# Performance work log

Measured on AMD Instinct MI355X. Metric: run time of the kernel, lower is better.

Reference implementation:

```python
import jax, jax.numpy as jnp
import numpy as np

B, S, D, H = 2, 2048, 1024, 16  # batch, pad_size, depth, num_heads
HD = D // H


def setup_inputs() -> dict:
    key = jax.random.key(0)
    ks = jax.random.split(key, 20)
    g = lambda k, shape, fan: jax.random.normal(k, shape, jnp.float32) * np.sqrt(2.0 / fan)
    return {
        "x": jax.random.normal(ks[0], (B, S, D), jnp.float32),
        "W_in": g(ks[1], (D, D), 2 * D), "b_in": g(ks[2], (D,), D),
        "Wq": g(ks[3], (D, D), 2 * D), "bq": g(ks[4], (D,), D),
        "Wk": g(ks[5], (D, D), 2 * D), "bk": g(ks[6], (D,), D),
        "Wv": g(ks[7], (D, D), 2 * D), "bv": g(ks[8], (D,), D),
        "Wo": g(ks[9], (D, D), 2 * D), "bo": g(ks[10], (D,), D),
        "W1": g(ks[11], (D, D), 2 * D), "b1": g(ks[12], (D,), D),
        "W2": g(ks[13], (D, D), 2 * D), "b2": g(ks[14], (D,), D),
        # residual gate scalars (random_id_att / random_id_ff); zero-init in the
        # original, set nonzero here so the whole graph contributes.
        "s_att": jax.random.normal(ks[15], (), jnp.float32),
        "s_ff": jax.random.normal(ks[16], (), jnp.float32),
    }


def reference(x, W_in, b_in, Wq, bq, Wk, bk, Wv, bv, Wo, bo, W1, b1, W2, b2, s_att, s_ff):
    # input projection
    h = x @ W_in + b_in                                   # [B,S,D]
    # QKV projections, split heads -> [B,H,S,HD]
    def heads(t):
        return t.reshape(B, S, H, HD).transpose(0, 2, 1, 3)
    q = heads(h @ Wq + bq)
    k = heads(h @ Wk + bk)
    v = heads(h @ Wv + bv)
    # attention: sigmoid(logits) * tanh(logits) instead of softmax
    logits = jnp.einsum("bhqd,bhkd->bhqk", q, k) / jnp.sqrt(jnp.float32(D))
    attn = jax.nn.sigmoid(logits) * jnp.tanh(logits)      # [B,H,S,S]
    ctx = jnp.einsum("bhqk,bhkd->bhqd", attn, v)
    ctx = ctx.transpose(0, 2, 1, 3).reshape(B, S, D)
    attention = ctx @ Wo + bo
    # gated residual 1
    latent = h + s_att * attention
    # FFN (depth -> depth -> depth), leaky_relu alpha=0.2 (tf default);
    # dropout treated as identity (inference)
    ff = jax.nn.leaky_relu(latent @ W1 + b1, negative_slope=0.2) @ W2 + b2
    out = latent + s_ff * ff
    return out
```

## Files before the change

### kernel.cpp

```cpp
#include <hip/hip_runtime.h>
#include <cstdint>
#include <cstddef>


#define B_ 2
#define S_ 2048
#define D_ 1024
#define H_ 16
#define M_ 4096

typedef __attribute__((ext_vector_type(4))) float  f32x4;
typedef __attribute__((ext_vector_type(8))) __bf16 bf16x8;
typedef __attribute__((ext_vector_type(4))) __bf16 bf16x4;

#define WAITVM(N) asm volatile("s_waitcnt vmcnt(" #N ")" ::: "memory")

__device__ __forceinline__ void async16(const void* g, void* l) {
    __builtin_amdgcn_global_load_lds(
        (__attribute__((address_space(1))) void*)(g),
        (__attribute__((address_space(3))) void*)(l), 16, 0, 0);
}

__device__ __forceinline__ float actf(float s) {
    float t = fminf(s * -0.045084223f, 21.6f);
    float u = __builtin_amdgcn_exp2f(t);
    return (1.f - u) * __builtin_amdgcn_rcpf(1.f + u * u);
}

template <int EPI>
__global__ __launch_bounds__(256) void gemm_k(
    const __bf16* __restrict__ A, const __bf16* __restrict__ Bt,
    const float* __restrict__ bias, const __bf16* __restrict__ aux,
    const float* __restrict__ scal, void* __restrict__ out, int Ntot)
{
    constexpr int K = D_;
    __shared__ __align__(16) __bf16 As[2][128][64];
    __shared__ __align__(16) __bf16 Bs[2][64][64];

    const int tid = threadIdx.x, lane = tid & 63, wid = tid >> 6;
    const int wr = wid >> 1, wc = wid & 1;
    const int cpx = (int)gridDim.x >> 3;
    const int bid = (int)blockIdx.x;
    const int wg = (bid & 7) * cpx + (bid >> 3);
    const int m0 = (wg & 31) * 128;
    const int n0 = (wg >> 5) * 64;
    const int frow = lane & 15;
    const int kb = (lane >> 4) * 16;
    char* cAs = (char*)As; char* cBs = (char*)Bs;

    f32x4 acc[4][2] = {};

    auto stage = [&](int buf, int k0) {
#pragma unroll
        for (int i = 0; i < 4; ++i) {
            const int o = tid * 16 + i * 4096;
            const int row = o >> 7;
            const int cb = (o & 127) ^ ((row & 7) << 4);
            async16(A + (size_t)(m0 + row) * K + k0 + (cb >> 1),
                    cAs + buf * 16384 + o);
        }
#pragma unroll
        for (int i = 0; i < 2; ++i) {
            const int o = tid * 16 + i * 4096;
            const int row = o >> 7;
            const int cb = (o & 127) ^ ((row & 7) << 4);
            async16(Bt + (size_t)(n0 + row) * K + k0 + (cb >> 1),
                    cBs + buf * 8192 + o);
        }
    };

    auto compute = [&](int buf) {
        char* lA = cAs + buf * 16384;
        char* lB = cBs + buf * 8192;
#pragma unroll
        for (int kk = 0; kk < 2; ++kk) {
            bf16x8 af[4], bfr[2];
#pragma unroll
            for (int m = 0; m < 4; ++m) {
                const int r = wr * 64 + m * 16 + frow;
                af[m] = *(const bf16x8*)(lA + ((r * 128 + kk * 64 + kb) ^ ((r & 7) << 4)));
            }
#pragma unroll
            for (int n = 0; n < 2; ++n) {
                const int r = wc * 32 + n * 16 + frow;
                bfr[n] = *(const bf16x8*)(lB + ((r * 128 + kk * 64 + kb) ^ ((r & 7) << 4)));
            }
#pragma unroll
            for (int m = 0; m < 4; ++m)
#pragma unroll
                for (int n = 0; n < 2; ++n)
                    acc[m][n] = __builtin_amdgcn_mfma_f32_16x16x32_bf16(
                        af[m], bfr[n], acc[m][n], 0, 0, 0);
        }
    };

    stage(0, 0);
    stage(1, 64);
    WAITVM(6);
    __builtin_amdgcn_sched_barrier(0);
    __builtin_amdgcn_s_barrier();

    for (int tp = 0; tp < 8; ++tp) {
        const int t0 = tp * 2;
        compute(0);
        __builtin_amdgcn_s_barrier();
        if (t0 < 14) { stage(0, (t0 + 2) * 64); WAITVM(6); }
        else         { WAITVM(0); }
        __builtin_amdgcn_sched_barrier(0);
        __builtin_amdgcn_s_barrier();
        compute(1);
        __builtin_amdgcn_s_barrier();
        if (t0 < 14) { stage(1, (t0 + 3) * 64); WAITVM(6); }
        __builtin_amdgcn_sched_barrier(0);
        __builtin_amdgcn_s_barrier();
    }

    const float sv = (EPI >= 2) ? *scal : 0.f;
#pragma unroll
    for (int m = 0; m < 4; ++m) {
#pragma unroll
        for (int n = 0; n < 2; ++n) {
#pragma unroll
            for (int r = 0; r < 4; ++r) {
                const int row = m0 + wr * 64 + m * 16 + (lane >> 4) * 4 + r;
                const int col = n0 + wc * 32 + n * 16 + frow;
                const size_t idx = (size_t)row * Ntot + col;
                float v = acc[m][n][r] + bias[col];
                if constexpr (EPI == 0) {
                    ((__bf16*)out)[idx] = (__bf16)v;
                } else if constexpr (EPI == 1) {
                    v = v > 0.f ? v : 0.2f * v;
                    ((__bf16*)out)[idx] = (__bf16)v;
                } else if constexpr (EPI == 2) {
                    ((__bf16*)out)[idx] = (__bf16)((float)aux[idx] + sv * v);
                } else {
                    ((float*)out)[idx] = (float)aux[idx] + sv * v;
                }
            }
        }
    }
}

__global__ __launch_bounds__(256, 4) void attn_k(
    const __bf16* __restrict__ Q, const __bf16* __restrict__ Kmat,
    const __bf16* __restrict__ VT, __bf16* __restrict__ CTX, int ld)
{
    __shared__ __align__(16) __bf16 Ks[2][64][64];
    __shared__ __align__(16) __bf16 Vs[2][64][64];
    __shared__ __align__(16) __bf16 Ps[64][64];

    const int tid = threadIdx.x, wid = tid >> 6, lane = tid & 63;
    const int bid = (int)blockIdx.x;
    const int wg = (bid & 7) * 128 + (bid >> 3);
    const int qt = wg & 31, h = (wg >> 5) & 15, b = wg >> 9;
    const int q0 = qt * 64;
    const int frow = lane & 15, g = lane >> 4;
    const int kg8 = g * 8, kb = g * 16;
    const int qrow = wid * 16 + frow;

    const __bf16* qbase = Q    + (size_t)(b * S_ + q0) * ld + h * 64;
    const __bf16* kbase = Kmat + (size_t)b * S_ * ld + h * 64;
    const __bf16* vbase = VT   + (size_t)(b * H_ + h) * 64 * S_;

    bf16x8 qf[2];
#pragma unroll
    for (int kk = 0; kk < 2; ++kk)
        qf[kk] = *(const bf16x8*)(qbase + (size_t)qrow * ld + kk * 32 + kg8);
    __builtin_amdgcn_sched_barrier(0);

    f32x4 octx[4] = {};
    char* cKs = (char*)Ks; char* cVs = (char*)Vs; char* lPs = (char*)Ps;

    auto stageKV = [&](int buf, int kt) {
#pragma unroll
        for (int i = 0; i < 2; ++i) {
            const int o = tid * 16 + i * 4096;
            const int row = o >> 7;
            const int cb = (o & 127) ^ ((row & 7) << 4);
            async16(kbase + (size_t)(kt + row) * ld + (cb >> 1),
                    cKs + buf * 8192 + o);
            async16(vbase + (size_t)row * S_ + kt + (cb >> 1),
                    cVs + buf * 8192 + o);
        }
    };

    auto computeTile = [&](char* lKs, char* lVs) {
        f32x4 scc[4] = {};
        __builtin_amdgcn_s_setprio(1);
#pragma unroll
        for (int kk = 0; kk < 2; ++kk) {
            bf16x8 kf[4];
#pragma unroll
            for (int n = 0; n < 4; ++n) {
                const int r = n * 16 + frow;
                kf[n] = *(const bf16x8*)(lKs + ((r * 128 + kk * 64 + kb) ^ ((r & 7) << 4)));
            }
#pragma unroll
            for (int n = 0; n < 4; ++n)
                scc[n] = __builtin_amdgcn_mfma_f32_16x16x32_bf16(
                    kf[n], qf[kk], scc[n], 0, 0, 0);
        }
        __builtin_amdgcn_s_setprio(0);
#pragma unroll
        for (int n = 0; n < 4; ++n) {
            bf16x4 pw;
#pragma unroll
            for (int r = 0; r < 4; ++r) pw[r] = (__bf16)actf(scc[n][r]);
            *(bf16x4*)(lPs + ((qrow * 128 + n * 32 + g * 8) ^ ((qrow & 7) << 4))) = pw;
        }
        __builtin_amdgcn_s_setprio(1);
#pragma unroll
        for (int ks = 0; ks < 2; ++ks) {
            bf16x8 pf = *(const bf16x8*)(lPs +
                ((qrow * 128 + ks * 64 + kb) ^ ((qrow & 7) << 4)));
            bf16x8 vf[4];
#pragma unroll
            for (int nd = 0; nd < 4; ++nd) {
                const int rd = nd * 16 + frow;
                vf[nd] = *(const bf16x8*)(lVs + ((rd * 128 + ks * 64 + kb) ^ ((rd & 7) << 4)));
            }
#pragma unroll
            for (int nd = 0; nd < 4; ++nd)
                octx[nd] = __builtin_amdgcn_mfma_f32_16x16x32_bf16(
                    pf, vf[nd], octx[nd], 0, 0, 0);
        }
        __builtin_amdgcn_s_setprio(0);
    };

    stageKV(0, 0);
    stageKV(1, 64);
    WAITVM(4);
    __builtin_amdgcn_sched_barrier(0);
    __builtin_amdgcn_s_barrier();

    for (int it = 0; it < 16; ++it) {
        const int kt0 = it * 128;
        computeTile(cKs, cVs);
        __builtin_amdgcn_s_barrier();
        if (it < 15) { stageKV(0, kt0 + 128); WAITVM(4); }
        else         { WAITVM(0); }
        __builtin_amdgcn_sched_barrier(0);
        __builtin_amdgcn_s_barrier();
        computeTile(cKs + 8192, cVs + 8192);
        __builtin_amdgcn_s_barrier();
        if (it < 15) { stageKV(1, kt0 + 192); WAITVM(4); }
        __builtin_amdgcn_sched_barrier(0);
        __builtin_amdgcn_s_barrier();
    }

#pragma unroll
    for (int nd = 0; nd < 4; ++nd)
#pragma unroll
        for (int r = 0; r < 4; ++r) {
            const int row = q0 + wid * 16 + g * 4 + r;
            const int col = h * 64 + nd * 16 + frow;
            CTX[(size_t)(b * S_ + row) * D_ + col] = (__bf16)octx[nd][r];
        }
}

struct WPack { const float* w[7]; };

__global__ __launch_bounds__(256) void conv_transpose_w(WPack p, __bf16* out) {
    __shared__ float t[32][33];
    const float* W = p.w[blockIdx.z];
    __bf16* o = out + (size_t)blockIdx.z * D_ * D_;
    const int c0 = blockIdx.x * 32, r0 = blockIdx.y * 32;
    const int tx = threadIdx.x, ty = threadIdx.y;
#pragma unroll
    for (int i = 0; i < 4; ++i)
        t[ty + i * 8][tx] = W[(size_t)(r0 + ty + i * 8) * D_ + c0 + tx];
    __syncthreads();
#pragma unroll
    for (int i = 0; i < 4; ++i)
        o[(size_t)(c0 + ty + i * 8) * D_ + r0 + tx] = (__bf16)t[tx][ty + i * 8];
}

__global__ __launch_bounds__(256) void conv_bf16(
    const float* __restrict__ in, __bf16* __restrict__ out, int n4)
{
    const int i = blockIdx.x * blockDim.x + threadIdx.x;
    if (i < n4) {
        f32x4 v = ((const f32x4*)in)[i];
        bf16x4 o;
        o[0] = (__bf16)v[0]; o[1] = (__bf16)v[1];
        o[2] = (__bf16)v[2]; o[3] = (__bf16)v[3];
        ((bf16x4*)out)[i] = o;
    }
}

__global__ __launch_bounds__(256) void bcat_k(
    const float* __restrict__ bq, const float* __restrict__ bk,
    const float* __restrict__ bv, float* __restrict__ o)
{
    const int i = blockIdx.x * 256 + threadIdx.x;
    o[i] = i < 1024 ? bq[i] : (i < 2048 ? bk[i - 1024] : bv[i - 2048]);
}

__global__ __launch_bounds__(256) void transpose_v(
    const __bf16* __restrict__ V, __bf16* __restrict__ VT, int ld)
{
    __shared__ __bf16 t[32][33];
    const int s0 = blockIdx.x * 32, c0 = blockIdx.y * 32, b = blockIdx.z;
    const int tx = threadIdx.x, ty = threadIdx.y;
#pragma unroll
    for (int i = 0; i < 4; ++i)
        t[ty + i * 8][tx] = V[(size_t)(b * S_ + s0 + ty + i * 8) * ld + c0 + tx];
    __syncthreads();
#pragma unroll
    for (int i = 0; i < 4; ++i)
        VT[(size_t)(b * D_ + c0 + ty + i * 8) * S_ + s0 + tx] = t[tx][ty + i * 8];
}

extern "C" void kernel_launch(void* const* d_in, const int* in_sizes, int n_in,
                              void* d_out, int out_size, void* d_ws, size_t ws_size,
                              hipStream_t stream) {
    const float* x    = (const float*)d_in[0];
    const float* W_in = (const float*)d_in[1];
    const float* b_in = (const float*)d_in[2];
    const float* Wq   = (const float*)d_in[3];
    const float* bq   = (const float*)d_in[4];
    const float* Wk   = (const float*)d_in[5];
    const float* bk   = (const float*)d_in[6];
    const float* Wv   = (const float*)d_in[7];
    const float* bv   = (const float*)d_in[8];
    const float* Wo   = (const float*)d_in[9];
    const float* bo   = (const float*)d_in[10];
    const float* W1   = (const float*)d_in[11];
    const float* b1   = (const float*)d_in[12];
    const float* W2   = (const float*)d_in[13];
    const float* b2   = (const float*)d_in[14];
    const float* s_att = (const float*)d_in[15];
    const float* s_ff  = (const float*)d_in[16];

    char* ws = (char*)d_ws;
    const size_t WB = (size_t)D_ * D_ * 2;
    const size_t MB = (size_t)M_ * D_ * 2;
    __bf16* WT   = (__bf16*)(ws);
    __bf16* Hb   = (__bf16*)(ws + 7 * WB);
    __bf16* QKVb = (__bf16*)(ws + 7 * WB + MB);
    __bf16* VTb  = (__bf16*)(ws + 7 * WB + 4 * MB);
    __bf16* Xb   = (__bf16*)(ws + 7 * WB + 5 * MB);
    float*  bcat = (float*)VTb;
    __bf16* CTXb = Xb;
    __bf16* LATb = QKVb;
    __bf16* FF1b = QKVb + (size_t)M_ * D_;
    auto WTi = [&](int i) { return WT + (size_t)i * D_ * D_; };

    WPack wp;
    wp.w[0] = W_in; wp.w[1] = Wq; wp.w[2] = Wk; wp.w[3] = Wv;
    wp.w[4] = Wo;   wp.w[5] = W1; wp.w[6] = W2;
    conv_transpose_w<<<dim3(32, 32, 7), dim3(32, 8), 0, stream>>>(wp, WT);
    conv_bf16<<<dim3(4096), dim3(256), 0, stream>>>(x, Xb, (M_ * D_) / 4);
    bcat_k<<<dim3(12), dim3(256), 0, stream>>>(bq, bk, bv, bcat);

    gemm_k<0><<<dim3(512), dim3(256), 0, stream>>>(
        Xb, WTi(0), b_in, nullptr, nullptr, Hb, D_);
    gemm_k<0><<<dim3(1536), dim3(256), 0, stream>>>(
        Hb, WTi(1), bcat, nullptr, nullptr, QKVb, 3 * D_);
    transpose_v<<<dim3(64, 32, 2), dim3(32, 8), 0, stream>>>(
        QKVb + 2 * D_, VTb, 3 * D_);
    attn_k<<<dim3(1024), dim3(256), 0, stream>>>(
        QKVb, QKVb + D_, VTb, CTXb, 3 * D_);
    gemm_k<2><<<dim3(512), dim3(256), 0, stream>>>(
        CTXb, WTi(4), bo, Hb, s_att, LATb, D_);
    gemm_k<1><<<dim3(512), dim3(256), 0, stream>>>(
        LATb, WTi(5), b1, nullptr, nullptr, FF1b, D_);
    gemm_k<3><<<dim3(512), dim3(256), 0, stream>>>(
        FF1b, WTi(6), b2, LATb, s_ff, d_out, D_);
}
```

Before: 289.6 us.

## Split attention key range across warps with LDS reduction, retile GEMM grid order

The attention kernel now handles 32 query rows per block, and each of the four warps processes a disjoint quarter of the key sequence. Each warp has its own double-buffered K/V staging and no block-wide barriers inside the loop. Partial context accumulators are combined through LDS float atomics before one vectorized store. This removes per-tile block barriers and doubles the grid, at the cost of more LDS per block (lower occupancy bound) and an extra reduction. The GEMM now takes the N-tile count as a compile-time parameter, swaps the M/N tile ordering so consecutive workgroups share A rows, and adds a min-blocks launch bound.

```diff
diff --git a/kernel.cpp b/kernel.cpp
--- a/kernel.cpp
+++ b/kernel.cpp
@@ -27,13 +27,14 @@
     return (1.f - u) * __builtin_amdgcn_rcpf(1.f + u * u);
 }
 
-template <int EPI>
-__global__ __launch_bounds__(256) void gemm_k(
+template <int EPI, int NT>
+__global__ __launch_bounds__(256, 3) void gemm_k(
     const __bf16* __restrict__ A, const __bf16* __restrict__ Bt,
     const float* __restrict__ bias, const __bf16* __restrict__ aux,
-    const float* __restrict__ scal, void* __restrict__ out, int Ntot)
+    const float* __restrict__ scal, void* __restrict__ out)
 {
     constexpr int K = D_;
+    constexpr int Ntot = NT * 64;
     __shared__ __align__(16) __bf16 As[2][128][64];
     __shared__ __align__(16) __bf16 Bs[2][64][64];
 
@@ -42,8 +43,8 @@
     const int cpx = (int)gridDim.x >> 3;
     const int bid = (int)blockIdx.x;
     const int wg = (bid & 7) * cpx + (bid >> 3);
-    const int m0 = (wg & 31) * 128;
-    const int n0 = (wg >> 5) * 64;
+    const int m0 = (wg / NT) * 128;
+    const int n0 = (wg % NT) * 64;
     const int frow = lane & 15;
     const int kb = (lane >> 4) * 16;
     char* cAs = (char*)As; char* cBs = (char*)Bs;
@@ -141,121 +142,149 @@
     }
 }
 
-__global__ __launch_bounds__(256, 4) void attn_k(
+__global__ __launch_bounds__(256, 2) void attn_k(
     const __bf16* __restrict__ Q, const __bf16* __restrict__ Kmat,
     const __bf16* __restrict__ VT, __bf16* __restrict__ CTX, int ld)
 {
-    __shared__ __align__(16) __bf16 Ks[2][64][64];
-    __shared__ __align__(16) __bf16 Vs[2][64][64];
-    __shared__ __align__(16) __bf16 Ps[64][64];
+    __shared__ __align__(16) char smem[81920];
+    char* cK = smem;
+    char* cV = smem + 32768;
+    char* cP = smem + 65536;
+    float* sAcc = (float*)(smem + 73728);
 
     const int tid = threadIdx.x, wid = tid >> 6, lane = tid & 63;
     const int bid = (int)blockIdx.x;
-    const int wg = (bid & 7) * 128 + (bid >> 3);
-    const int qt = wg & 31, h = (wg >> 5) & 15, b = wg >> 9;
-    const int q0 = qt * 64;
+    const int wg = (bid & 7) * 256 + (bid >> 3);
+    const int qt = wg & 63, h = (wg >> 6) & 15, b = wg >> 10;
+    const int q0 = qt * 32;
     const int frow = lane & 15, g = lane >> 4;
-    const int kg8 = g * 8, kb = g * 16;
-    const int qrow = wid * 16 + frow;
+    const int kg8 = g * 8;
 
     const __bf16* qbase = Q    + (size_t)(b * S_ + q0) * ld + h * 64;
     const __bf16* kbase = Kmat + (size_t)b * S_ * ld + h * 64;
     const __bf16* vbase = VT   + (size_t)(b * H_ + h) * 64 * S_;
 
-    bf16x8 qf[2];
-#pragma unroll
-    for (int kk = 0; kk < 2; ++kk)
-        qf[kk] = *(const bf16x8*)(qbase + (size_t)qrow * ld + kk * 32 + kg8);
+#pragma unroll
+    for (int i = 0; i < 2; ++i)
+        ((f32x4*)sAcc)[tid + i * 256] = f32x4{0.f, 0.f, 0.f, 0.f};
+    __syncthreads();
+
+    bf16x8 qf[2][2];
+#pragma unroll
+    for (int qf_ = 0; qf_ < 2; ++qf_)
+#pragma unroll
+        for (int kk = 0; kk < 2; ++kk)
+            qf[qf_][kk] = *(const bf16x8*)(qbase +
+                (size_t)(16 * qf_ + frow) * ld + kk * 32 + kg8);
     __builtin_amdgcn_sched_barrier(0);
 
-    f32x4 octx[4] = {};
-    char* cKs = (char*)Ks; char* cVs = (char*)Vs; char* lPs = (char*)Ps;
-
-    auto stageKV = [&](int buf, int kt) {
-#pragma unroll
-        for (int i = 0; i < 2; ++i) {
-            const int o = tid * 16 + i * 4096;
+    auto stK = [&](int buf, int kt) {
+#pragma unroll
+        for (int i = 0; i < 4; ++i) {
+            const int o = lane * 16 + i * 1024;
             const int row = o >> 7;
             const int cb = (o & 127) ^ ((row & 7) << 4);
             async16(kbase + (size_t)(kt + row) * ld + (cb >> 1),
-                    cKs + buf * 8192 + o);
+                    cK + wid * 8192 + buf * 4096 + o);
+        }
+    };
+    auto stV = [&](int buf, int kt) {
+#pragma unroll
+        for (int i = 0; i < 4; ++i) {
+            const int o = lane * 16 + i * 1024;
+            const int row = o >> 6;
+            const int cb = (o & 63) ^ ((row & 3) << 4);
             async16(vbase + (size_t)row * S_ + kt + (cb >> 1),
-                    cVs + buf * 8192 + o);
+                    cV + wid * 8192 + buf * 4096 + o);
         }
     };
 
-    auto computeTile = [&](char* lKs, char* lVs) {
-        f32x4 scc[4] = {};
-        __builtin_amdgcn_s_setprio(1);
-#pragma unroll
-        for (int kk = 0; kk < 2; ++kk) {
-            bf16x8 kf[4];
-#pragma unroll
-            for (int n = 0; n < 4; ++n) {
-                const int r = n * 16 + frow;
-                kf[n] = *(const bf16x8*)(lKs + ((r * 128 + kk * 64 + kb) ^ ((r & 7) << 4)));
-            }
-#pragma unroll
-            for (int n = 0; n < 4; ++n)
-                scc[n] = __builtin_amdgcn_mfma_f32_16x16x32_bf16(
-                    kf[n], qf[kk], scc[n], 0, 0, 0);
-        }
-        __builtin_amdgcn_s_setprio(0);
-#pragma unroll
-        for (int n = 0; n < 4; ++n) {
-            bf16x4 pw;
-#pragma unroll
-            for (int r = 0; r < 4; ++r) pw[r] = (__bf16)actf(scc[n][r]);
-            *(bf16x4*)(lPs + ((qrow * 128 + n * 32 + g * 8) ^ ((qrow & 7) << 4))) = pw;
-        }
-        __builtin_amdgcn_s_setprio(1);
-#pragma unroll
-        for (int ks = 0; ks < 2; ++ks) {
-            bf16x8 pf = *(const bf16x8*)(lPs +
-                ((qrow * 128 + ks * 64 + kb) ^ ((qrow & 7) << 4)));
-            bf16x8 vf[4];
-#pragma unroll
-            for (int nd = 0; nd < 4; ++nd) {
-                const int rd = nd * 16 + frow;
-                vf[nd] = *(const bf16x8*)(lVs + ((rd * 128 + ks * 64 + kb) ^ ((rd & 7) << 4)));
-            }
-#pragma unroll
-            for (int nd = 0; nd < 4; ++nd)
-                octx[nd] = __builtin_amdgcn_mfma_f32_16x16x32_bf16(
-                    pf, vf[nd], octx[nd], 0, 0, 0);
-        }
-        __builtin_amdgcn_s_setprio(0);
-    };
-
-    stageKV(0, 0);
-    stageKV(1, 64);
-    WAITVM(4);
-    __builtin_amdgcn_sched_barrier(0);
-    __builtin_amdgcn_s_barrier();
-
-    for (int it = 0; it < 16; ++it) {
-        const int kt0 = it * 128;
-        computeTile(cKs, cVs);
-        __builtin_amdgcn_s_barrier();
-        if (it < 15) { stageKV(0, kt0 + 128); WAITVM(4); }
-        else         { WAITVM(0); }
+    const int kt0 = wid * 32;
+    stK(0, kt0);        stV(0, kt0);
+    stK(1, kt0 + 128);  stV(1, kt0 + 128);
+    WAITVM(8);
+
+    f32x4 acc[2][4] = {};
+
+    for (int t = 0; t < 16; ++t) {
+        char* bK = cK + wid * 8192 + (t & 1) * 4096;
+        char* bV = cV + wid * 8192 + (t & 1) * 4096;
+        char* bP = cP + wid * 2048;
+
+        f32x4 scc[2][2] = {};
+#pragma unroll
+        for (int kk = 0; kk < 2; ++kk)
+#pragma unroll
+            for (int kf_ = 0; kf_ < 2; ++kf_) {
+                const int row = 16 * kf_ + frow;
+                bf16x8 kfv = *(const bf16x8*)(bK +
+                    (row * 128 + ((kk * 64 + g * 16) ^ ((row & 7) << 4))));
+#pragma unroll
+                for (int qf_ = 0; qf_ < 2; ++qf_)
+                    scc[kf_][qf_] = __builtin_amdgcn_mfma_f32_16x16x32_bf16(
+                        kfv, qf[qf_][kk], scc[kf_][qf_], 0, 0, 0);
+            }
+
+#pragma unroll
+        for (int kf_ = 0; kf_ < 2; ++kf_)
+#pragma unroll
+            for (int qf_ = 0; qf_ < 2; ++qf_) {
+                bf16x4 pw;
+#pragma unroll
+                for (int r = 0; r < 4; ++r) pw[r] = (__bf16)actf(scc[kf_][qf_][r]);
+                const int row = 16 * qf_ + frow;
+                *(bf16x4*)(bP + row * 64 +
+                    ((kf_ * 32 + g * 8) ^ ((row & 3) << 4))) = pw;
+            }
+
+        bf16x8 pa[2], vf[4];
+#pragma unroll
+        for (int qf_ = 0; qf_ < 2; ++qf_) {
+            const int row = 16 * qf_ + frow;
+            pa[qf_] = *(const bf16x8*)(bP + row * 64 +
+                ((g * 16) ^ ((row & 3) << 4)));
+        }
+#pragma unroll
+        for (int df = 0; df < 4; ++df) {
+            const int row = 16 * df + frow;
+            vf[df] = *(const bf16x8*)(bV + row * 64 +
+                ((g * 16) ^ ((row & 3) << 4)));
+        }
+        asm volatile("s_waitcnt lgkmcnt(0)" ::: "memory");
         __builtin_amdgcn_sched_barrier(0);
-        __builtin_amdgcn_s_barrier();
-        computeTile(cKs + 8192, cVs + 8192);
-        __builtin_amdgcn_s_barrier();
-        if (it < 15) { stageKV(1, kt0 + 192); WAITVM(4); }
-        __builtin_amdgcn_sched_barrier(0);
-        __builtin_amdgcn_s_barrier();
-    }
-
-#pragma unroll
-    for (int nd = 0; nd < 4; ++nd)
-#pragma unroll
-        for (int r = 0; r < 4; ++r) {
-            const int row = q0 + wid * 16 + g * 4 + r;
-            const int col = h * 64 + nd * 16 + frow;
-            CTX[(size_t)(b * S_ + row) * D_ + col] = (__bf16)octx[nd][r];
-        }
+        if (t < 14) {
+            stK(t & 1, kt0 + (t + 2) * 128);
+            stV(t & 1, kt0 + (t + 2) * 128);
+        }
+#pragma unroll
+        for (int qf_ = 0; qf_ < 2; ++qf_)
+#pragma unroll
+            for (int df = 0; df < 4; ++df)
+                acc[qf_][df] = __builtin_amdgcn_mfma_f32_16x16x32_bf16(
+                    pa[qf_], vf[df], acc[qf_][df], 0, 0, 0);
+        if (t < 14) { WAITVM(8); }
+        else        { WAITVM(0); }
+    }
+
+#pragma unroll
+    for (int qf_ = 0; qf_ < 2; ++qf_)
+#pragma unroll
+        for (int df = 0; df < 4; ++df)
+#pragma unroll
+            for (int r = 0; r < 4; ++r)
+                atomicAdd(&sAcc[(16 * qf_ + 4 * g + r) * 64 + 16 * df + frow],
+                          acc[qf_][df][r]);
+    __syncthreads();
+#pragma unroll
+    for (int i = 0; i < 2; ++i) {
+        const int idx4 = (tid + i * 256) * 4;
+        const int q = idx4 >> 6, dc = idx4 & 63;
+        f32x4 v = *(const f32x4*)&sAcc[idx4];
+        bf16x4 o4;
+        o4[0] = (__bf16)v[0]; o4[1] = (__bf16)v[1];
+        o4[2] = (__bf16)v[2]; o4[3] = (__bf16)v[3];
+        *(bf16x4*)&CTX[(size_t)(b * S_ + q0 + q) * D_ + h * 64 + dc] = o4;
+    }
 }
 
 struct WPack { const float* w[7]; };
@@ -353,18 +382,18 @@
     conv_bf16<<<dim3(4096), dim3(256), 0, stream>>>(x, Xb, (M_ * D_) / 4);
     bcat_k<<<dim3(12), dim3(256), 0, stream>>>(bq, bk, bv, bcat);
 
-    gemm_k<0><<<dim3(512), dim3(256), 0, stream>>>(
-        Xb, WTi(0), b_in, nullptr, nullptr, Hb, D_);
-    gemm_k<0><<<dim3(1536), dim3(256), 0, stream>>>(
-        Hb, WTi(1), bcat, nullptr, nullptr, QKVb, 3 * D_);
+    gemm_k<0, 16><<<dim3(512), dim3(256), 0, stream>>>(
+        Xb, WTi(0), b_in, nullptr, nullptr, Hb);
+    gemm_k<0, 48><<<dim3(1536), dim3(256), 0, stream>>>(
+        Hb, WTi(1), bcat, nullptr, nullptr, QKVb);
     transpose_v<<<dim3(64, 32, 2), dim3(32, 8), 0, stream>>>(
         QKVb + 2 * D_, VTb, 3 * D_);
-    attn_k<<<dim3(1024), dim3(256), 0, stream>>>(
+    attn_k<<<dim3(2048), dim3(256), 0, stream>>>(
         QKVb, QKVb + D_, VTb, CTXb, 3 * D_);
-    gemm_k<2><<<dim3(512), dim3(256), 0, stream>>>(
-        CTXb, WTi(4), bo, Hb, s_att, LATb, D_);
-    gemm_k<1><<<dim3(512), dim3(256), 0, stream>>>(
-        LATb, WTi(5), b1, nullptr, nullptr, FF1b, D_);
-    gemm_k<3><<<dim3(512), dim3(256), 0, stream>>>(
-        FF1b, WTi(6), b2, LATb, s_ff, d_out, D_);
-}
+    gemm_k<2, 16><<<dim3(512), dim3(256), 0, stream>>>(
+        CTXb, WTi(4), bo, Hb, s_att, LATb);
+    gemm_k<1, 16><<<dim3(512), dim3(256), 0, stream>>>(
+        LATb, WTi(5), b1, nullptr, nullptr, FF1b);
+    gemm_k<3, 16><<<dim3(512), dim3(256), 0, stream>>>(
+        FF1b, WTi(6), b2, LATb, s_ff, d_out);
+}
```

After: 371.3 us. 28.2% more time.
